# Kernel optimization log

Measured on AMD Instinct MI355X. Metric: run time of the kernel, lower is better.

## Reference

```python
import jax, jax.numpy as jnp
import numpy as np

B = 128; Hm = 13; Wm = 13; P = Hm * Wm; D = 256; TC = 32; RH = 512; EPS = 1e-5
START_TILE = 31


def _ln(x, g, b):
    m = jnp.mean(x, -1, keepdims=True)
    v = jnp.mean((x - m) ** 2, -1, keepdims=True)
    return (x - m) * jax.lax.rsqrt(v + EPS) * g + b


def _gelu(x):
    return jax.nn.gelu(x, approximate=False)


def _fwd(target_map, map_vec, mv_w, mv_b, tile_emb, row_emb, col_emb, pos_w, pos_b,
         c1_w, c1_b, bn1_g, bn1_b, c2_w, c2_b, bn2_g, bn2_b, patch_fc_w, patch_fc_b,
         qkv_w, qkv_b, out_w, out_b, ln1_g, ln1_b, ff1_w, ff1_b, ff2_w, ff2_b,
         ln2_g, ln2_b, gru_wih, gru_whh, gru_bih, gru_bhh,
         fc1_w, fc1_b, fcln_g, fcln_b, fc2_w, fc2_b):
    Bn = map_vec.shape[0]
    ys = jnp.arange(P) // Wm
    xs = jnp.arange(P) % Wm
    d5 = jnp.arange(5)
    # map_vec projection [B,256]
    mv = map_vec @ mv_w.T + mv_b
    # positional embedding for all 169 positions: cat(row_emb[y], col_emb[x]) -> fusion
    pos = jnp.concatenate([row_emb[ys], col_emb[xs]], -1) @ pos_w.T + pos_b  # [P,256]
    # teacher-forced previous tile (use_self_probility=0 path)
    tflat = target_map.reshape(Bn, P)
    prev = jnp.concatenate([jnp.full((Bn, 1), START_TILE, tflat.dtype), tflat[:, :-1]], 1)
    te = tile_emb[prev]  # [B,P,256]
    # 5x5 causal patches: rows y-4..y, cols x-2..x+2, out-of-bounds + current/future-on-row masked
    padded = jnp.pad(target_map, ((0, 0), (4, 0), (2, 2)))  # [B,17,17]
    rows = ys[:, None] + d5
    cols = xs[:, None] + d5
    patch = padded[:, rows[:, :, None], cols[:, None, :]]  # [B,P,5,5]
    vr = (ys[:, None, None] - 4 + d5[None, :, None]) >= 0
    oc = xs[:, None, None] - 2 + d5[None, None, :]
    vc = (oc >= 0) & (oc < Wm)
    mask = (vr & vc)
    mask = mask.at[:, 4, 2:].set(False)  # zero current cell and the two to its right
    patch = jnp.where(mask[None], patch, 0)
    oh = jax.nn.one_hot(patch, TC, dtype=jnp.float32)  # [B,P,row,col,c]
    # torch: permute(0,3,2,1) transposes the spatial dims of the one-hot channels
    ch = jnp.transpose(oh, (0, 1, 4, 3, 2))  # [B,P,32,col,row]
    mch = jnp.broadcast_to(mask.astype(jnp.float32)[None, :, None], (Bn, P, 1, 5, 5))
    x = jnp.concatenate([ch, mch], 2).reshape(Bn * P, TC + 1, 5, 5)
    dn = ('NCHW', 'OIHW', 'NCHW')
    bnsc = 1.0 / np.sqrt(1.0 + EPS)  # eval BN with running mean 0 / var 1
    x = jax.lax.conv_general_dilated(x, c1_w, (1, 1), 'SAME', dimension_numbers=dn) + c1_b[None, :, None, None]
    x = _gelu(x * (bn1_g * bnsc)[None, :, None, None] + bn1_b[None, :, None, None])
    x = jax.lax.conv_general_dilated(x, c2_w, (1, 1), 'VALID', dimension_numbers=dn) + c2_b[None, :, None, None]
    x = _gelu(x * (bn2_g * bnsc)[None, :, None, None] + bn2_b[None, :, None, None])
    pf = x.reshape(Bn * P, 128 * 9) @ patch_fc_w.T + patch_fc_b  # [B*P,256]
    # fusion transformer over 4 tokens, batched across all 169 steps
    tok = jnp.stack([
        te.reshape(Bn * P, D),
        jnp.broadcast_to(mv[:, None], (Bn, P, D)).reshape(Bn * P, D),
        jnp.broadcast_to(pos[None], (Bn, P, D)).reshape(Bn * P, D),
        pf], 1)  # [B*P,4,256]
    h = tok
    for l in range(3):  # post-norm encoder layers, relu FFN, dropout=0 at eval
        qkv = h @ qkv_w[l].T + qkv_b[l]
        q, k, v = jnp.split(qkv, 3, -1)
        hd = lambda t: t.reshape(-1, 4, 2, 128).transpose(0, 2, 1, 3)  # 2 heads of 128
        q, k, v = hd(q), hd(k), hd(v)
        a = jax.nn.softmax(jnp.einsum('nhqd,nhkd->nhqk', q, k) / np.sqrt(128.0), -1)
        o = jnp.einsum('nhqk,nhkd->nhqd', a, v).transpose(0, 2, 1, 3).reshape(-1, 4, D)
        h = _ln(h + o @ out_w[l].T + out_b[l], ln1_g[l], ln1_b[l])
        ff = jax.nn.relu(h @ ff1_w[l].T + ff1_b[l]) @ ff2_w[l].T + ff2_b[l]
        h = _ln(h + ff, ln2_g[l], ln2_b[l])
    feat = h[:, 0].reshape(Bn, P, D).transpose(1, 0, 2)  # [P,B,256]
    # GRUCell recurrence over the 169 raster steps
    gi = feat @ gru_wih.T + gru_bih  # [P,B,1536]

    def step(hid, g):
        gh = hid @ gru_whh.T + gru_bhh
        ir, iz, inn = jnp.split(g, 3, -1)
        hr, hz, hn = jnp.split(gh, 3, -1)
        r = jax.nn.sigmoid(ir + hr)
        z = jax.nn.sigmoid(iz + hz)
        n = jnp.tanh(inn + r * hn)
        hid = (1 - z) * n + z * hid
        return hid, hid

    _, hs = jax.lax.scan(step, jnp.zeros((Bn, RH), jnp.float32), gi)  # [P,B,512]
    hs = hs.transpose(1, 0, 2)  # [B,P,512]
    y = _gelu(_ln(hs @ fc1_w.T + fc1_b, fcln_g, fcln_b))
    logits = y @ fc2_w.T + fc2_b  # [B,P,32]
    return logits.reshape(Bn, Hm, Wm, TC).transpose(0, 3, 1, 2)  # [B,32,13,13]


def setup_inputs() -> dict:
    key = jax.random.key(0)
    ks = jax.random.split(key, 24)
    r = lambda i, s: jax.random.normal(ks[i], s, jnp.float32) * 0.02
    return {
        'map_vec': jax.random.normal(ks[0], (B, 32), jnp.float32),
        'target_map': jax.random.randint(ks[1], (B, Hm, Wm), 0, TC, jnp.int32),
        'mv_w': r(2, (256, 32)), 'mv_b': jnp.zeros(256),
        'tile_emb': r(3, (32, 256)),
        'row_emb': r(4, (13, 256)), 'col_emb': r(5, (13, 256)),
        'pos_w': r(6, (256, 512)), 'pos_b': jnp.zeros(256),
        'c1_w': r(7, (64, 33, 3, 3)), 'c1_b': jnp.zeros(64),
        'bn1_g': jnp.ones(64), 'bn1_b': jnp.zeros(64),
        'c2_w': r(8, (128, 64, 3, 3)), 'c2_b': jnp.zeros(128),
        'bn2_g': jnp.ones(128), 'bn2_b': jnp.zeros(128),
        'patch_fc_w': r(9, (256, 1152)), 'patch_fc_b': jnp.zeros(256),
        'qkv_w': r(10, (3, 768, 256)), 'qkv_b': jnp.zeros((3, 768)),
        'out_w': r(11, (3, 256, 256)), 'out_b': jnp.zeros((3, 256)),
        'ln1_g': jnp.ones((3, 256)), 'ln1_b': jnp.zeros((3, 256)),
        'ff1_w': r(12, (3, 256, 256)), 'ff1_b': jnp.zeros((3, 256)),
        'ff2_w': r(13, (3, 256, 256)), 'ff2_b': jnp.zeros((3, 256)),
        'ln2_g': jnp.ones((3, 256)), 'ln2_b': jnp.zeros((3, 256)),
        'gru_wih': r(14, (1536, 256)), 'gru_whh': r(15, (1536, 512)),
        'gru_bih': jnp.zeros(1536), 'gru_bhh': jnp.zeros(1536),
        'fc1_w': r(16, (512, 512)), 'fc1_b': jnp.zeros(512),
        'fcln_g': jnp.ones(512), 'fcln_b': jnp.zeros(512),
        'fc2_w': r(17, (32, 512)), 'fc2_b': jnp.zeros(32),
    }


def reference(map_vec, target_map, mv_w, mv_b, tile_emb, row_emb, col_emb, pos_w, pos_b,
              c1_w, c1_b, bn1_g, bn1_b, c2_w, c2_b, bn2_g, bn2_b, patch_fc_w, patch_fc_b,
              qkv_w, qkv_b, out_w, out_b, ln1_g, ln1_b, ff1_w, ff1_b, ff2_w, ff2_b,
              ln2_g, ln2_b, gru_wih, gru_whh, gru_bih, gru_bhh,
              fc1_w, fc1_b, fcln_g, fcln_b, fc2_w, fc2_b):
    return _fwd(target_map, map_vec, mv_w, mv_b, tile_emb, row_emb, col_emb, pos_w, pos_b,
                c1_w, c1_b, bn1_g, bn1_b, c2_w, c2_b, bn2_g, bn2_b, patch_fc_w, patch_fc_b,
                qkv_w, qkv_b, out_w, out_b, ln1_g, ln1_b, ff1_w, ff1_b, ff2_w, ff2_b,
                ln2_g, ln2_b, gru_wih, gru_whh, gru_bih, gru_bhh,
                fc1_w, fc1_b, fcln_g, fcln_b, fc2_w, fc2_b)
```

## Files before the change

### kernel.cpp

```cpp
#include <hip/hip_runtime.h>
#include <hip/hip_bf16.h>

typedef unsigned short u16;
typedef unsigned char u8;
typedef unsigned int u32;
typedef __attribute__((ext_vector_type(8))) short bf16x8;
typedef __attribute__((ext_vector_type(4))) float f32x4;
typedef __attribute__((ext_vector_type(4))) unsigned int u32x4;

__device__ __forceinline__ float us2f(u16 u){ return __uint_as_float(((unsigned)u)<<16); }
__device__ __forceinline__ u16 f2us(float f){
  __hip_bfloat16 h = __float2bfloat16(f);
  union { __hip_bfloat16 b; u16 s; } cv; cv.b = h; return cv.s;
}
__device__ __forceinline__ float gelu_f(float v){ return 0.5f*v*(1.f+erff(v*0.70710678118654752f)); }
__device__ __forceinline__ float sigm_f(float v){ return 1.f/(1.f+expf(-v)); }

#define BNSC 0.9999950000374997f

struct PrepArgs {
  const float *qkv_w, *out_w, *ff1_w, *ff2_w, *g_wih, *fc1_w, *pf_w, *c2_w, *fc2_w, *fc2_b;
  const float *c1_w, *c1_b, *bn2_g;
  const float *map_vec, *mv_w, *mv_b, *row_e, *col_e, *pos_w, *pos_b;
  const int *tm;
  u16 *qkvw_d, *outw_d, *ff1w_d, *ff2w_d, *wihw_d, *fc1w_d, *pfw_d, *w2k_d, *fc2w_d;
  float *fc2b_d, *w1t_d, *t2_d, *s2_d, *mv_d, *pos_d;
  u8 *ecls_d;
  unsigned *bar;
};
#define SB_QKV 2304
#define SB_O   768
#define SB_WIH 1536
#define SB_FC1 1024
#define SB_PF  1152
#define SB_W2  288
#define SB_FC2 128
#define SB_W1T 72
#define SB_T2  1057
#define SB_MV  128
#define SB_POS 169
#define SB_EC  2113
#define PREP_GRID (1+SB_QKV+3*SB_O+SB_WIH+SB_FC1+SB_PF+SB_W2+SB_FC2+SB_W1T+SB_T2+SB_MV+SB_POS+SB_EC)

__global__ __launch_bounds__(256) void prep_kernel(PrepArgs a){
  int bb = blockIdx.x; const int tid = threadIdx.x;
  if (bb < 1){
    if (tid < 64)  a.bar[tid] = 0u;
    if (tid < 128) a.s2_d[tid] = a.bn2_g[tid]*BNSC;
    return;
  } bb -= 1;
  if (bb < SB_QKV){ int i = bb*256+tid; a.qkvw_d[i] = f2us(a.qkv_w[i]); return; } bb -= SB_QKV;
  if (bb < SB_O){ int i = bb*256+tid; a.outw_d[i] = f2us(a.out_w[i]); return; } bb -= SB_O;
  if (bb < SB_O){ int i = bb*256+tid; a.ff1w_d[i] = f2us(a.ff1_w[i]); return; } bb -= SB_O;
  if (bb < SB_O){ int i = bb*256+tid; a.ff2w_d[i] = f2us(a.ff2_w[i]); return; } bb -= SB_O;
  if (bb < SB_WIH){ int i = bb*256+tid; a.wihw_d[i] = f2us(a.g_wih[i]); return; } bb -= SB_WIH;
  if (bb < SB_FC1){ int i = bb*256+tid; a.fc1w_d[i] = f2us(a.fc1_w[i]); return; } bb -= SB_FC1;
  if (bb < SB_PF){
    int i = bb*256+tid;
    int o = i/1152, kp = i%1152, pos = kp>>7, c = kp&127;
    a.pfw_d[i] = f2us(a.pf_w[o*1152 + c*9 + pos]); return;
  } bb -= SB_PF;
  if (bb < SB_W2){
    int i = bb*256+tid;
    int o = i/576, k = i%576, tap = k>>6, ic = k&63, ty = tap/3, tx = tap%3;
    a.w2k_d[i] = f2us(a.c2_w[((o*64 + ic)*3 + ty)*3 + tx]); return;
  } bb -= SB_W2;
  if (bb < SB_FC2){
    int i = bb*256+tid;
    int o = i>>9, k = i&511;
    a.fc2w_d[i] = (o<32) ? f2us(a.fc2_w[o*512+k]) : (u16)0;
    if (i < 64) a.fc2b_d[i] = (i<32) ? a.fc2_b[i] : 0.f;
    return;
  } bb -= SB_FC2;
  if (bb < SB_W1T){
    int i = bb*256+tid;
    int c = i/576, r = i%576, tap = r>>6, o = r&63;
    a.w1t_d[i] = a.c1_w[(o*33 + c)*9 + tap]; return;
  } bb -= SB_W1T;
  if (bb < SB_T2){
    int i = bb*256+tid; if (i >= 169*25*64) return;
    int blk = i/64, o = i%64;
    int p = blk/25, op = blk%25, oy = op/5, ox = op%5;
    int yp = p/13, xp = p%13;
    float acc = a.c1_b[o];
    for (int dy=0; dy<3; dy++) for (int dx=0; dx<3; dx++){
      int Y = oy+dy-1, X = ox+dx-1;
      if (Y<0||Y>4||X<0||X>4) continue;
      int rr = yp + Y - 4, cc = xp + X - 2;
      bool m = (rr>=0) && (cc>=0) && (cc<13) && !(Y==4 && X>=2);
      if (m) acc += a.c1_w[(o*33 + 32)*9 + dy*3 + dx];
    }
    a.t2_d[((long)p*25 + op)*64 + o] = acc; return;
  } bb -= SB_T2;
  if (bb < SB_MV){
    int i = bb*256+tid;
    int bi = i>>8, o = i&255;
    float acc = a.mv_b[o];
    for (int k=0;k<32;k++) acc += a.map_vec[bi*32+k]*a.mv_w[o*32+k];
    a.mv_d[i] = acc; return;
  } bb -= SB_MV;
  if (bb < SB_POS){
    int i = bb*256+tid;
    int p = i>>8, o = i&255;
    int y = p/13, x = p%13;
    const float* wr = a.pos_w + o*512;
    float acc = a.pos_b[o];
    for (int k=0;k<256;k++) acc += a.row_e[y*256+k]*wr[k];
    for (int k=0;k<256;k++) acc += a.col_e[x*256+k]*wr[256+k];
    a.pos_d[i] = acc; return;
  } bb -= SB_POS;
  {
    int id = bb*256+tid; if (id >= 21632*25) return;
    int n = id/25, q = id%25, Y = q/5, X = q%5;
    int b = n/169, p = n%169, yp = p/13, xp = p%13;
    int rr = yp + X - 4, cc = xp + Y - 2;
    int val = 0;
    if (rr>=0 && cc>=0 && cc<13 && !(X==4 && Y>=2)) val = a.tm[b*169 + rr*13 + cc];
    a.ecls_d[id] = (u8)val;
  }
}

__global__ __launch_bounds__(256) void conv1_kernel(
    const u8* __restrict__ ec, const float* __restrict__ w1t, const float* __restrict__ t2,
    const float* __restrict__ bn1g, const float* __restrict__ bn1b, u16* __restrict__ c1out,
    int nbase){
  __shared__ __align__(16) u16 w1s[32*9*64];
  __shared__ u8 ecs[32*25];
  const int tid = threadIdx.x, nl0 = blockIdx.x*32;
  for (int i=tid; i<32*9*64; i+=256) w1s[i] = f2us(w1t[i]);
  for (int i=tid; i<32*25;   i+=256) ecs[i] = ec[((long)nbase + nl0)*25 + i];
  __syncthreads();
  const int grp = tid>>6, o = tid&63;
  const float s1 = bn1g[o]*BNSC, t1 = bn1b[o];
  for (int it = grp; it < 800; it += 4){
    const int nl = it/25, op = it%25, oy = op/5, ox = op%5;
    const int n = nbase + nl0 + nl, p = n%169;
    float acc = t2[((long)p*25 + op)*64 + o];
    #pragma unroll
    for (int dy=0; dy<3; dy++)
      #pragma unroll
      for (int dx=0; dx<3; dx++){
        int Y = oy+dy-1, X = ox+dx-1;
        if (Y>=0 && Y<5 && X>=0 && X<5){
          int e = ecs[nl*25 + Y*5 + X];
          acc += us2f(w1s[(e*9 + dy*3+dx)*64 + o]);
        }
      }
    c1out[((long)(nl0+nl)*25 + op)*64 + o] = f2us(gelu_f(acc*s1 + t1));
  }
}

template<int NT, int OM>
__global__ __launch_bounds__(256) void gemm_bt(
    const u16* A, long lda, const u16* __restrict__ W,
    const float* __restrict__ bias,
    float* outF, u16* outB, long ldc, int N, int K, int act,
    const u16* __restrict__ lbase, const float* __restrict__ lg, const float* __restrict__ lb){
  __shared__ __align__(16) u16 As[64][72];
  __shared__ __align__(16) u16 Ws[NT][64][72];
  const int tid = threadIdx.x, wv = tid>>6, lane = tid&63;
  const int quad = lane>>4, l16 = lane&15;
  const int bm = blockIdx.y, bn = blockIdx.x;
  f32x4 acc[NT*4];
  #pragma unroll
  for (int i=0;i<NT*4;i++) acc[i] = (f32x4){0.f,0.f,0.f,0.f};
  const int sm = tid>>2, sk = (tid&3)<<4;
  const long arow = (long)(bm*64 + sm)*lda;
  for (int kb = 0; kb < K; kb += 64){
    int4 a0 = *(const int4*)(A + arow + kb + sk);
    int4 a1 = *(const int4*)(A + arow + kb + sk + 8);
    *(int4*)&As[sm][sk]   = a0;  *(int4*)&As[sm][sk+8] = a1;
    #pragma unroll
    for (int wt=0; wt<NT; wt++){
      const long wrow = (long)(bn*(64*NT) + wt*64 + sm)*K;
      int4 w0 = *(const int4*)(W + wrow + kb + sk);
      int4 w1 = *(const int4*)(W + wrow + kb + sk + 8);
      *(int4*)&Ws[wt][sm][sk]   = w0;  *(int4*)&Ws[wt][sm][sk+8] = w1;
    }
    __syncthreads();
    #pragma unroll
    for (int ks = 0; ks < 64; ks += 32){
      bf16x8 af = *(const bf16x8*)(&As[wv*16 + l16][ks + quad*8]);
      #pragma unroll
      for (int wt=0; wt<NT; wt++)
        #pragma unroll
        for (int s=0; s<4; s++){
          bf16x8 bfv = *(const bf16x8*)(&Ws[wt][s*16 + l16][ks + quad*8]);
          acc[wt*4+s] = __builtin_amdgcn_mfma_f32_16x16x32_bf16(af, bfv, acc[wt*4+s], 0, 0, 0);
        }
    }
    __syncthreads();
  }
  const int mb = bm*64 + wv*16 + quad*4;
  if (OM == 2){
    #pragma unroll
    for (int wt=0; wt<NT; wt++)
      #pragma unroll
      for (int s=0; s<4; s++){
        const int n = wt*64 + s*16 + l16;
        const float bv = bias[n];
        #pragma unroll
        for (int r=0;r<4;r++)
          acc[wt*4+s][r] = acc[wt*4+s][r] + bv + us2f(lbase[(long)(mb+r)*N + n]);
      }
    float mean[4], rstd[4];
    #pragma unroll
    for (int r=0;r<4;r++){
      float s = 0.f;
      #pragma unroll
      for (int i=0;i<NT*4;i++) s += acc[i][r];
      s += __shfl_xor(s,1); s += __shfl_xor(s,2); s += __shfl_xor(s,4); s += __shfl_xor(s,8);
      mean[r] = s / N;
      float v = 0.f;
      #pragma unroll
      for (int i=0;i<NT*4;i++){ float d = acc[i][r]-mean[r]; v += d*d; }
      v += __shfl_xor(v,1); v += __shfl_xor(v,2); v += __shfl_xor(v,4); v += __shfl_xor(v,8);
      rstd[r] = rsqrtf(v/N + 1e-5f);
    }
    #pragma unroll
    for (int wt=0; wt<NT; wt++)
      #pragma unroll
      for (int s=0; s<4; s++){
        const int n = wt*64 + s*16 + l16;
        const float gv = lg[n], bvv = lb[n];
        #pragma unroll
        for (int r=0;r<4;r++)
          outB[(long)(mb+r)*ldc + n] = f2us((acc[wt*4+s][r]-mean[r])*rstd[r]*gv + bvv);
      }
    return;
  }
  #pragma unroll
  for (int wt=0; wt<NT; wt++)
    #pragma unroll
    for (int s=0; s<4; s++){
      const int n = bn*(64*NT) + wt*64 + s*16 + l16;
      const float bv = bias ? bias[n] : 0.f;
      #pragma unroll
      for (int r=0;r<4;r++){
        float v = acc[wt*4+s][r] + bv;
        if (act==1) v = fmaxf(v, 0.f);
        else if (act==2) v = gelu_f(v);
        if (OM == 1){
          const int m = mb + r, b = m/169, tt = m%169;
          const int gate = n>>9, cblk = (n>>4)&31, jl = n&15;
          outB[(((long)tt*32 + cblk)*3 + gate)*2048 + b*16 + jl] = f2us(v);
        } else if (OM == 3){
          if (n < 32){
            const int m = mb + r, t = m/128, b2 = m%128;
            outF[((long)b2*32 + n)*169 + t] = v;
          }
        } else {
          const long oo = (long)(mb + r)*ldc + n;
          if (outF) outF[oo] = v;
          if (outB) outB[oo] = f2us(v);
        }
      }
    }
}

__global__ __launch_bounds__(256) void gemm_conv2(
    const u16* __restrict__ C1, const u16* __restrict__ W,
    const float* __restrict__ bias, const float* __restrict__ scale, const float* __restrict__ shift,
    u16* __restrict__ outB){
  __shared__ __align__(16) u16 As[64][72];
  __shared__ __align__(16) u16 Ws[64][72];
  const int tid = threadIdx.x, wv = tid>>6, lane = tid&63;
  const int quad = lane>>4, l16 = lane&15;
  const int bm = blockIdx.y, bn = blockIdx.x;
  f32x4 acc[4];
  #pragma unroll
  for (int i=0;i<4;i++) acc[i] = (f32x4){0.f,0.f,0.f,0.f};
  const int sm = tid>>2, sk = (tid&3)<<4;
  const int g = bm*64 + sm, n_ = g/9, pos = g%9, py = pos/3, px = pos%3;
  const long wrow = (long)(bn*64 + sm)*576;
  for (int tap = 0; tap < 9; tap++){
    const int kb = tap*64;
    const long aoff = ((long)n_*25 + (py + tap/3)*5 + (px + tap%3))*64 + sk;
    int4 a0 = *(const int4*)(C1 + aoff);
    int4 a1 = *(const int4*)(C1 + aoff + 8);
    int4 w0 = *(const int4*)(W + wrow + kb + sk);
    int4 w1 = *(const int4*)(W + wrow + kb + sk + 8);
    *(int4*)&As[sm][sk]   = a0;  *(int4*)&As[sm][sk+8] = a1;
    *(int4*)&Ws[sm][sk]   = w0;  *(int4*)&Ws[sm][sk+8] = w1;
    __syncthreads();
    #pragma unroll
    for (int ks = 0; ks < 64; ks += 32){
      bf16x8 af = *(const bf16x8*)(&As[wv*16 + l16][ks + quad*8]);
      #pragma unroll
      for (int nt=0; nt<4; nt++){
        bf16x8 bfv = *(const bf16x8*)(&Ws[nt*16 + l16][ks + quad*8]);
        acc[nt] = __builtin_amdgcn_mfma_f32_16x16x32_bf16(af, bfv, acc[nt], 0, 0, 0);
      }
    }
    __syncthreads();
  }
  const int mb = bm*64 + wv*16 + quad*4;
  #pragma unroll
  for (int nt=0; nt<4; nt++){
    const int n = bn*64 + nt*16 + l16;
    const float bv = bias[n], sc = scale[n], sh = shift[n];
    #pragma unroll
    for (int r=0;r<4;r++){
      float v = (acc[nt][r] + bv)*sc + sh;
      outB[(long)(mb + r)*128 + n] = f2us(gelu_f(v));
    }
  }
}

__global__ void token_kernel(const int* __restrict__ tm, const float* __restrict__ te,
                             const float* __restrict__ mv, const float* __restrict__ pos,
                             u16* __restrict__ hB){
  const int n = blockIdx.x, k = threadIdx.x;
  const int b = n/169, p = n%169;
  const int prev = (p==0) ? 31 : tm[b*169 + p - 1];
  const long r0 = (long)n*1024;
  hB[r0 + k]        = f2us(te[prev*256 + k]);
  hB[r0 + 256 + k]  = f2us(mv[b*256 + k]);
  hB[r0 + 512 + k]  = f2us(pos[p*256 + k]);
}

__global__ __launch_bounds__(256) void attn_kernel(const u16* __restrict__ qkv, u16* o){
  const int n = blockIdx.x*4 + (threadIdx.x>>6);
  const int lane = threadIdx.x & 63;
  float qv[4][2][2], kv[4][2][2], vv[4][2][2];
  #pragma unroll
  for (int tok=0; tok<4; tok++){
    const long rb = (long)(n*4+tok)*768;
    #pragma unroll
    for (int h=0; h<2; h++){
      unsigned u;
      u = *(const unsigned*)(qkv + rb +        h*128 + 2*lane); qv[tok][h][0]=us2f(u&0xffff); qv[tok][h][1]=us2f(u>>16);
      u = *(const unsigned*)(qkv + rb + 256 +  h*128 + 2*lane); kv[tok][h][0]=us2f(u&0xffff); kv[tok][h][1]=us2f(u>>16);
      u = *(const unsigned*)(qkv + rb + 512 +  h*128 + 2*lane); vv[tok][h][0]=us2f(u&0xffff); vv[tok][h][1]=us2f(u>>16);
    }
  }
  float sc[2][4][4];
  #pragma unroll
  for (int h=0; h<2; h++)
    #pragma unroll
    for (int qt=0; qt<4; qt++)
      #pragma unroll
      for (int kt=0; kt<4; kt++){
        float p_ = qv[qt][h][0]*kv[kt][h][0] + qv[qt][h][1]*kv[kt][h][1];
        for (int off=32; off; off>>=1) p_ += __shfl_xor(p_, off);
        sc[h][qt][kt] = p_ * 0.08838834764831845f;
      }
  #pragma unroll
  for (int h=0; h<2; h++)
    #pragma unroll
    for (int qt=0; qt<4; qt++){
      float m = fmaxf(fmaxf(sc[h][qt][0],sc[h][qt][1]),fmaxf(sc[h][qt][2],sc[h][qt][3]));
      float s = 0.f;
      #pragma unroll
      for (int kt=0; kt<4; kt++){ sc[h][qt][kt] = expf(sc[h][qt][kt]-m); s += sc[h][qt][kt]; }
      float inv = 1.f/s;
      #pragma unroll
      for (int kt=0; kt<4; kt++) sc[h][qt][kt] *= inv;
    }
  #pragma unroll
  for (int qt=0; qt<4; qt++)
    #pragma unroll
    for (int h=0; h<2; h++){
      float o0=0.f, o1=0.f;
      #pragma unroll
      for (int kt=0; kt<4; kt++){ o0 += sc[h][qt][kt]*vv[kt][h][0]; o1 += sc[h][qt][kt]*vv[kt][h][1]; }
      unsigned u = (unsigned)f2us(o0) | ((unsigned)f2us(o1)<<16);
      *(unsigned*)(o + (long)(n*4+qt)*256 + h*128 + 2*lane) = u;
    }
}

template<int NPL>
__global__ __launch_bounds__(256) void ln_kernel(
    const u16* __restrict__ delta, const u16* __restrict__ base,
    const float* __restrict__ g, const float* __restrict__ b,
    u16* __restrict__ out, int do_gelu){
  const int D = NPL*64;
  const int row = blockIdx.x*4 + (threadIdx.x>>6);
  const int lane = threadIdx.x & 63;
  const long ro = (long)row*D;
  float x[NPL];
  float s = 0.f;
  #pragma unroll
  for (int i=0;i<NPL;i++){
    float v = us2f(delta[ro + i*64 + lane]);
    if (base) v += us2f(base[ro + i*64 + lane]);
    x[i] = v; s += v;
  }
  for (int off=32; off; off>>=1) s += __shfl_xor(s, off);
  const float mean = s / D;
  float var = 0.f;
  #pragma unroll
  for (int i=0;i<NPL;i++){ float dd = x[i]-mean; var += dd*dd; }
  for (int off=32; off; off>>=1) var += __shfl_xor(var, off);
  const float rs = rsqrtf(var/D + 1e-5f);
  #pragma unroll
  for (int i=0;i<NPL;i++){
    float y = (x[i]-mean)*rs*g[i*64+lane] + b[i*64+lane];
    if (do_gelu) y = gelu_f(y);
    out[ro + i*64 + lane] = f2us(y);
  }
}

__global__ __launch_bounds__(256) void gru_kernel(
    const u16* __restrict__ gix, const float* __restrict__ whh,
    const float* __restrict__ bhh, u16* __restrict__ hx, u16* __restrict__ hs,
    unsigned* __restrict__ bar){
  __shared__ __align__(16) u16 Wl[48][520];
  __shared__ __align__(16) u16 hbuf[2048];
  const int c = blockIdx.x, tid = threadIdx.x;
  const int wv = tid>>6, lane = tid&63, quad = lane>>4, l16 = lane&15;
  for (int idx = tid; idx < 48*512; idx += 256){
    int g = idx >> 9, k = idx & 511;
    int gate = g >> 4, jl = g & 15;
    Wl[g][k] = f2us(whh[((gate<<9) + (c<<4) + jl)*512 + k]);
  }
  const int j = (c<<4) + l16;
  const float bh_r = bhh[j], bh_z = bhh[512+j], bh_n = bhh[1024+j];
  __syncthreads();
  float hold[2][4] = {{0.f,0.f,0.f,0.f},{0.f,0.f,0.f,0.f}};
  const int jlo = (quad&1)*8, jhiadd = quad>>1;
  for (int t=0; t<169; t++){
    const u16* gbase = gix + ((long)t*32 + c)*3*2048;
    float gr_[2][4], gz_[2][4], gn_[2][4];
    #pragma unroll
    for (int mt=0; mt<2; mt++)
      #pragma unroll
      for (int r=0; r<4; r++){
        const int b = (2*wv+mt)*16 + quad*4 + r;
        gr_[mt][r] = us2f(gbase[       b*16 + l16]);
        gz_[mt][r] = us2f(gbase[2048 + b*16 + l16]);
        gn_[mt][r] = us2f(gbase[4096 + b*16 + l16]);
      }
    if (t>0){
      if (tid==0){
        while (__hip_atomic_load(bar, __ATOMIC_RELAXED, __HIP_MEMORY_SCOPE_AGENT) < (unsigned)(32*t))
          __builtin_amdgcn_s_sleep(1);
      }
      __syncthreads();
    }
    f32x4 acc[2][3];
    #pragma unroll
    for (int mt=0; mt<2; mt++)
      #pragma unroll
      for (int g3=0; g3<3; g3++) acc[mt][g3] = (f32x4){0.f,0.f,0.f,0.f};
    if (t>0){
      const long tb = (long)(t-1)*65536;
      const int b0 = (2*wv+0)*16 + l16, b1 = (2*wv+1)*16 + l16;
      bf16x8 av0[16], av1[16];
      #pragma unroll
      for (int ii=0; ii<16; ii++){
        const long off = tb + (long)(ii*2 + jhiadd)*2048 + jlo;
        const u16* p0 = hx + off + b0*16;
        const u16* p1 = hx + off + b1*16;
        asm volatile("global_load_dwordx4 %0, %1, off sc0 sc1" : "=v"(av0[ii]) : "v"(p0));
        asm volatile("global_load_dwordx4 %0, %1, off sc0 sc1" : "=v"(av1[ii]) : "v"(p1));
      }
      asm volatile("s_waitcnt vmcnt(0)" ::: "memory");
      #pragma unroll
      for (int ii=0; ii<16; ii++){
        asm volatile("" : "+v"(av0[ii]));
        asm volatile("" : "+v"(av1[ii]));
      }
      #pragma unroll
      for (int ii=0; ii<16; ii++){
        const int ks = ii*32;
        #pragma unroll
        for (int g3=0; g3<3; g3++){
          bf16x8 bfv = *(const bf16x8*)(&Wl[g3*16 + l16][ks + quad*8]);
          acc[0][g3] = __builtin_amdgcn_mfma_f32_16x16x32_bf16(av0[ii], bfv, acc[0][g3], 0,0,0);
          acc[1][g3] = __builtin_amdgcn_mfma_f32_16x16x32_bf16(av1[ii], bfv, acc[1][g3], 0,0,0);
        }
      }
    }
    u16 hbv[2][4];
    #pragma unroll
    for (int mt=0; mt<2; mt++)
      #pragma unroll
      for (int r=0; r<4; r++){
        const int b = (2*wv+mt)*16 + quad*4 + r;
        float rr = sigm_f(gr_[mt][r] + acc[mt][0][r] + bh_r);
        float zz = sigm_f(gz_[mt][r] + acc[mt][1][r] + bh_z);
        float nn = tanhf (gn_[mt][r] + rr*(acc[mt][2][r] + bh_n));
        float h = (1.f-zz)*nn + zz*hold[mt][r];
        hold[mt][r] = h;
        hbv[mt][r] = f2us(h);
        hbuf[b*16 + l16] = hbv[mt][r];
      }
    __syncthreads();
    {
      u16* dst = hx + (long)t*65536 + c*2048 + tid*8;
      u32x4 val = *(const u32x4*)((const u32*)hbuf + tid*4);
      asm volatile("global_store_dwordx4 %0, %1, off sc0 sc1" :: "v"(dst), "v"(val) : "memory");
    }
    asm volatile("s_waitcnt vmcnt(0)" ::: "memory");
    __syncthreads();
    if (tid==0) __hip_atomic_fetch_add(bar, 1u, __ATOMIC_RELAXED, __HIP_MEMORY_SCOPE_AGENT);
    #pragma unroll
    for (int mt=0; mt<2; mt++)
      #pragma unroll
      for (int r=0; r<4; r++){
        const int b = (2*wv+mt)*16 + quad*4 + r;
        hs[((long)(t*128 + b))*512 + j] = hbv[mt][r];
      }
  }
}

extern "C" void kernel_launch(void* const* d_in, const int* in_sizes, int n_in,
                              void* d_out, int out_size, void* d_ws, size_t ws_size,
                              hipStream_t stream){
  (void)in_sizes; (void)n_in; (void)out_size;
  const float* map_vec = (const float*)d_in[0];
  const int*   tm      = (const int*)  d_in[1];
  const float* mv_w  = (const float*)d_in[2];
  const float* mv_b  = (const float*)d_in[3];
  const float* te    = (const float*)d_in[4];
  const float* row_e = (const float*)d_in[5];
  const float* col_e = (const float*)d_in[6];
  const float* pos_w = (const float*)d_in[7];
  const float* pos_b = (const float*)d_in[8];
  const float* c1_w  = (const float*)d_in[9];
  const float* c1_b  = (const float*)d_in[10];
  const float* bn1_g = (const float*)d_in[11];
  const float* bn1_b = (const float*)d_in[12];
  const float* c2_w  = (const float*)d_in[13];
  const float* c2_b  = (const float*)d_in[14];
  const float* bn2_g = (const float*)d_in[15];
  const float* bn2_b = (const float*)d_in[16];
  const float* pf_w  = (const float*)d_in[17];
  const float* pf_b  = (const float*)d_in[18];
  const float* qkv_w = (const float*)d_in[19];
  const float* qkv_b = (const float*)d_in[20];
  const float* out_w = (const float*)d_in[21];
  const float* out_b = (const float*)d_in[22];
  const float* ln1_g = (const float*)d_in[23];
  const float* ln1_b = (const float*)d_in[24];
  const float* ff1_w = (const float*)d_in[25];
  const float* ff1_b = (const float*)d_in[26];
  const float* ff2_w = (const float*)d_in[27];
  const float* ff2_b = (const float*)d_in[28];
  const float* ln2_g = (const float*)d_in[29];
  const float* ln2_b = (const float*)d_in[30];
  const float* g_wih = (const float*)d_in[31];
  const float* g_whh = (const float*)d_in[32];
  const float* g_bih = (const float*)d_in[33];
  const float* g_bhh = (const float*)d_in[34];
  const float* fc1_w = (const float*)d_in[35];
  const float* fc1_b = (const float*)d_in[36];
  const float* fln_g = (const float*)d_in[37];
  const float* fln_b = (const float*)d_in[38];
  const float* fc2_w = (const float*)d_in[39];
  const float* fc2_b = (const float*)d_in[40];

  char* ws = (char*)d_ws;
  constexpr size_t O_BAR  = 0;
  constexpr size_t O_QKVW = 256;
  constexpr size_t O_OUTW = O_QKVW + 1179648;
  constexpr size_t O_FF1W = O_OUTW + 393216;
  constexpr size_t O_FF2W = O_FF1W + 393216;
  constexpr size_t O_WIHW = O_FF2W + 393216;
  constexpr size_t O_FC1W = O_WIHW + 786432;
  constexpr size_t O_PFW  = O_FC1W + 524288;
  constexpr size_t O_W2K  = O_PFW  + 589824;
  constexpr size_t O_FC2W = O_W2K  + 147456;
  constexpr size_t O_FC2B = O_FC2W + 65536;
  constexpr size_t O_W1T  = O_FC2B + 256;
  constexpr size_t O_T2   = O_W1T  + 73728;
  constexpr size_t O_S2   = O_T2   + 1081600;
  constexpr size_t O_MV   = O_S2   + 512;
  constexpr size_t O_POS  = O_MV   + 131072;
  constexpr size_t O_ECLS = O_POS  + 173056;
  constexpr size_t O_R0   = ((O_ECLS + 540800 + 255)/256)*256;
  constexpr size_t R0_SZ  = 44302336;
  constexpr size_t O_R1   = O_R0 + R0_SZ;
  constexpr size_t R1_SZ  = 44302336;
  constexpr size_t O_R2   = O_R1 + R1_SZ;
  constexpr size_t R2_SZ  = 33226752;
  constexpr size_t ARENA_END = O_R2 + R2_SZ;
  if (ws_size < ARENA_END) return;
  const size_t O_HB    = O_R0;
  const size_t O_HX    = O_R0;
  const size_t O_HS    = O_R0 + 22151168;
  const size_t O_C1OUT = O_R1;
  const size_t O_OBUF  = O_R1;
  const size_t O_GIX   = O_R1;
  const size_t O_Y1    = O_R1;
  const size_t O_YB    = O_R1 + 22151168;
  const size_t O_C2OUT = O_R2;
  const size_t O_QKVC  = O_R2;

  PrepArgs pa;
  pa.qkv_w=qkv_w; pa.out_w=out_w; pa.ff1_w=ff1_w; pa.ff2_w=ff2_w; pa.g_wih=g_wih;
  pa.fc1_w=fc1_w; pa.pf_w=pf_w; pa.c2_w=c2_w; pa.fc2_w=fc2_w; pa.fc2_b=fc2_b;
  pa.c1_w=c1_w; pa.c1_b=c1_b; pa.bn2_g=bn2_g;
  pa.map_vec=map_vec; pa.mv_w=mv_w; pa.mv_b=mv_b; pa.row_e=row_e; pa.col_e=col_e;
  pa.pos_w=pos_w; pa.pos_b=pos_b; pa.tm=tm;
  pa.qkvw_d=(u16*)(ws+O_QKVW); pa.outw_d=(u16*)(ws+O_OUTW); pa.ff1w_d=(u16*)(ws+O_FF1W);
  pa.ff2w_d=(u16*)(ws+O_FF2W); pa.wihw_d=(u16*)(ws+O_WIHW); pa.fc1w_d=(u16*)(ws+O_FC1W);
  pa.pfw_d=(u16*)(ws+O_PFW); pa.w2k_d=(u16*)(ws+O_W2K); pa.fc2w_d=(u16*)(ws+O_FC2W);
  pa.fc2b_d=(float*)(ws+O_FC2B); pa.w1t_d=(float*)(ws+O_W1T); pa.t2_d=(float*)(ws+O_T2);
  pa.s2_d=(float*)(ws+O_S2); pa.mv_d=(float*)(ws+O_MV); pa.pos_d=(float*)(ws+O_POS);
  pa.ecls_d=(u8*)(ws+O_ECLS); pa.bar=(unsigned*)(ws+O_BAR);
  prep_kernel<<<PREP_GRID, 256, 0, stream>>>(pa);

  token_kernel<<<21632, 256, 0, stream>>>(tm, te, (const float*)(ws+O_MV), (const float*)(ws+O_POS),
      (u16*)(ws+O_HB));

  for (int cc = 0; cc < 2; cc++){
    const int nbase = cc*10816;
    conv1_kernel<<<338, 256, 0, stream>>>((const u8*)(ws+O_ECLS), (const float*)(ws+O_W1T),
        (const float*)(ws+O_T2), bn1_g, bn1_b, (u16*)(ws+O_C1OUT), nbase);
    gemm_conv2<<<dim3(2,1521), 256, 0, stream>>>((const u16*)(ws+O_C1OUT), (const u16*)(ws+O_W2K),
        c2_b, (const float*)(ws+O_S2), bn2_b, (u16*)(ws+O_C2OUT));
    gemm_bt<4,0><<<dim3(1,169), 256, 0, stream>>>((const u16*)(ws+O_C2OUT), 1152, (const u16*)(ws+O_PFW),
        pf_b, nullptr, (u16*)(ws+O_HB) + (size_t)nbase*1024 + 768, 1024, 256, 1152, 0,
        nullptr, nullptr, nullptr);
  }

  for (int l=0; l<3; l++){
    for (int cc = 0; cc < 4; cc++){
      gemm_bt<4,0><<<dim3(3,338), 256, 0, stream>>>((const u16*)(ws+O_HB) + (size_t)cc*21632*256, 256,
          (const u16*)(ws+O_QKVW) + (size_t)l*768*256, qkv_b + l*768,
          nullptr, (u16*)(ws+O_QKVC), 768, 768, 256, 0, nullptr, nullptr, nullptr);
      attn_kernel<<<1352, 256, 0, stream>>>((const u16*)(ws+O_QKVC),
          (u16*)(ws+O_OBUF) + (size_t)cc*5408*4*256);
    }
    gemm_bt<4,2><<<dim3(1,1352), 256, 0, stream>>>((const u16*)(ws+O_OBUF), 256,
        (const u16*)(ws+O_OUTW) + (size_t)l*256*256, out_b + l*256,
        nullptr, (u16*)(ws+O_HB), 256, 256, 256, 0,
        (const u16*)(ws+O_HB), ln1_g + l*256, ln1_b + l*256);
    gemm_bt<4,0><<<dim3(1,1352), 256, 0, stream>>>((const u16*)(ws+O_HB), 256,
        (const u16*)(ws+O_FF1W) + (size_t)l*256*256, ff1_b + l*256,
        nullptr, (u16*)(ws+O_OBUF), 256, 256, 256, 1, nullptr, nullptr, nullptr);
    gemm_bt<4,2><<<dim3(1,1352), 256, 0, stream>>>((const u16*)(ws+O_OBUF), 256,
        (const u16*)(ws+O_FF2W) + (size_t)l*256*256, ff2_b + l*256,
        nullptr, (u16*)(ws+O_HB), 256, 256, 256, 0,
        (const u16*)(ws+O_HB), ln2_g + l*256, ln2_b + l*256);
  }

  gemm_bt<4,1><<<dim3(6,338), 256, 0, stream>>>((const u16*)(ws+O_HB), 1024, (const u16*)(ws+O_WIHW),
      g_bih, nullptr, (u16*)(ws+O_GIX), 1536, 1536, 256, 0, nullptr, nullptr, nullptr);
  gru_kernel<<<32, 256, 0, stream>>>((const u16*)(ws+O_GIX), g_whh, g_bhh,
      (u16*)(ws+O_HX), (u16*)(ws+O_HS), (unsigned*)(ws+O_BAR));

  gemm_bt<4,0><<<dim3(2,338), 256, 0, stream>>>((const u16*)(ws+O_HS), 512, (const u16*)(ws+O_FC1W),
      fc1_b, nullptr, (u16*)(ws+O_Y1), 512, 512, 512, 0, nullptr, nullptr, nullptr);
  ln_kernel<8><<<5408, 256, 0, stream>>>((const u16*)(ws+O_Y1), nullptr, fln_g, fln_b,
      (u16*)(ws+O_YB), 1);
  gemm_bt<1,3><<<dim3(1,338), 256, 0, stream>>>((const u16*)(ws+O_YB), 512, (const u16*)(ws+O_FC2W),
      (const float*)(ws+O_FC2B), (float*)d_out, nullptr, 64, 64, 512, 0, nullptr, nullptr, nullptr);
}
```

Measured before the change: 2.921 ms.

## Use 128-row GEMM tiles and per-block flag barrier in GRU

Adds a gemm_bt2 variant that computes a 128x256 output tile per block (two M sub-tiles sharing each loaded weight fragment), halving grid size and weight reloads for the transformer, GRU input, and head GEMMs. The original gemm_bt is reduced to a plain bias-add kernel used only for the patch projection. The GRU inter-block barrier changes from a single atomic counter to per-block flag slots written with system-coherent stores and polled by 32 threads, which needs a larger zeroed barrier region. Larger tiles raise register pressure and may lower occupancy, and the flag protocol relies on cache-bypassing asm semantics.

```diff
diff --git a/kernel.cpp b/kernel.cpp
--- a/kernel.cpp
+++ b/kernel.cpp
@@ -45,7 +45,7 @@
 __global__ __launch_bounds__(256) void prep_kernel(PrepArgs a){
   int bb = blockIdx.x; const int tid = threadIdx.x;
   if (bb < 1){
-    if (tid < 64)  a.bar[tid] = 0u;
+    a.bar[tid] = 0u; a.bar[256+tid] = 0u;
     if (tid < 128) a.s2_d[tid] = a.bn2_g[tid]*BNSC;
     return;
   } bb -= 1;
@@ -150,12 +150,11 @@
   }
 }
 
-template<int NT, int OM>
+template<int NT>
 __global__ __launch_bounds__(256) void gemm_bt(
     const u16* A, long lda, const u16* __restrict__ W,
     const float* __restrict__ bias,
-    float* outF, u16* outB, long ldc, int N, int K, int act,
-    const u16* __restrict__ lbase, const float* __restrict__ lg, const float* __restrict__ lb){
+    u16* outB, long ldc, int N, int K){
   __shared__ __align__(16) u16 As[64][72];
   __shared__ __align__(16) u16 Ws[NT][64][72];
   const int tid = threadIdx.x, wv = tid>>6, lane = tid&63;
@@ -192,70 +191,139 @@
     __syncthreads();
   }
   const int mb = bm*64 + wv*16 + quad*4;
-  if (OM == 2){
-    #pragma unroll
-    for (int wt=0; wt<NT; wt++)
-      #pragma unroll
-      for (int s=0; s<4; s++){
-        const int n = wt*64 + s*16 + l16;
-        const float bv = bias[n];
-        #pragma unroll
-        for (int r=0;r<4;r++)
-          acc[wt*4+s][r] = acc[wt*4+s][r] + bv + us2f(lbase[(long)(mb+r)*N + n]);
-      }
-    float mean[4], rstd[4];
-    #pragma unroll
-    for (int r=0;r<4;r++){
-      float s = 0.f;
-      #pragma unroll
-      for (int i=0;i<NT*4;i++) s += acc[i][r];
-      s += __shfl_xor(s,1); s += __shfl_xor(s,2); s += __shfl_xor(s,4); s += __shfl_xor(s,8);
-      mean[r] = s / N;
-      float v = 0.f;
-      #pragma unroll
-      for (int i=0;i<NT*4;i++){ float d = acc[i][r]-mean[r]; v += d*d; }
-      v += __shfl_xor(v,1); v += __shfl_xor(v,2); v += __shfl_xor(v,4); v += __shfl_xor(v,8);
-      rstd[r] = rsqrtf(v/N + 1e-5f);
-    }
-    #pragma unroll
-    for (int wt=0; wt<NT; wt++)
-      #pragma unroll
-      for (int s=0; s<4; s++){
-        const int n = wt*64 + s*16 + l16;
-        const float gv = lg[n], bvv = lb[n];
-        #pragma unroll
-        for (int r=0;r<4;r++)
-          outB[(long)(mb+r)*ldc + n] = f2us((acc[wt*4+s][r]-mean[r])*rstd[r]*gv + bvv);
-      }
-    return;
-  }
   #pragma unroll
   for (int wt=0; wt<NT; wt++)
     #pragma unroll
     for (int s=0; s<4; s++){
       const int n = bn*(64*NT) + wt*64 + s*16 + l16;
-      const float bv = bias ? bias[n] : 0.f;
+      const float bv = bias[n];
+      #pragma unroll
+      for (int r=0;r<4;r++)
+        outB[(long)(mb + r)*ldc + n] = f2us(acc[wt*4+s][r] + bv);
+    }
+}
+
+template<int NT, int OM>
+__global__ __launch_bounds__(256) void gemm_bt2(
+    const u16* A, long lda, const u16* __restrict__ W,
+    const float* __restrict__ bias,
+    float* outF, u16* outB, long ldc, int N, int K, int act,
+    const u16* __restrict__ lbase, const float* __restrict__ lg, const float* __restrict__ lb){
+  __shared__ __align__(16) u16 As[128][72];
+  __shared__ __align__(16) u16 Ws[NT][64][72];
+  const int tid = threadIdx.x, wv = tid>>6, lane = tid&63;
+  const int quad = lane>>4, l16 = lane&15;
+  const int bm = blockIdx.y, bn = blockIdx.x;
+  f32x4 acc[2][NT*4];
+  #pragma unroll
+  for (int mt=0;mt<2;mt++)
+    #pragma unroll
+    for (int i=0;i<NT*4;i++) acc[mt][i] = (f32x4){0.f,0.f,0.f,0.f};
+  const int smA = tid>>1, skA = (tid&1)<<5;
+  const int smW = tid>>2, skW = (tid&3)<<4;
+  const long arow = (long)(bm*128 + smA)*lda;
+  for (int kb = 0; kb < K; kb += 64){
+    int4 a0 = *(const int4*)(A + arow + kb + skA);
+    int4 a1 = *(const int4*)(A + arow + kb + skA + 8);
+    int4 a2 = *(const int4*)(A + arow + kb + skA + 16);
+    int4 a3 = *(const int4*)(A + arow + kb + skA + 24);
+    *(int4*)&As[smA][skA]    = a0;  *(int4*)&As[smA][skA+8]  = a1;
+    *(int4*)&As[smA][skA+16] = a2;  *(int4*)&As[smA][skA+24] = a3;
+    #pragma unroll
+    for (int wt=0; wt<NT; wt++){
+      const long wrow = (long)(bn*(64*NT) + wt*64 + smW)*K;
+      int4 w0 = *(const int4*)(W + wrow + kb + skW);
+      int4 w1 = *(const int4*)(W + wrow + kb + skW + 8);
+      *(int4*)&Ws[wt][smW][skW]   = w0;  *(int4*)&Ws[wt][smW][skW+8] = w1;
+    }
+    __syncthreads();
+    #pragma unroll
+    for (int ks = 0; ks < 64; ks += 32){
+      bf16x8 af0 = *(const bf16x8*)(&As[wv*16 + l16][ks + quad*8]);
+      bf16x8 af1 = *(const bf16x8*)(&As[64 + wv*16 + l16][ks + quad*8]);
+      #pragma unroll
+      for (int wt=0; wt<NT; wt++)
+        #pragma unroll
+        for (int s=0; s<4; s++){
+          bf16x8 bfv = *(const bf16x8*)(&Ws[wt][s*16 + l16][ks + quad*8]);
+          acc[0][wt*4+s] = __builtin_amdgcn_mfma_f32_16x16x32_bf16(af0, bfv, acc[0][wt*4+s], 0, 0, 0);
+          acc[1][wt*4+s] = __builtin_amdgcn_mfma_f32_16x16x32_bf16(af1, bfv, acc[1][wt*4+s], 0, 0, 0);
+        }
+    }
+    __syncthreads();
+  }
+  if (OM == 2){
+    #pragma unroll
+    for (int mt=0; mt<2; mt++){
+      const int mb = bm*128 + mt*64 + wv*16 + quad*4;
+      #pragma unroll
+      for (int wt=0; wt<NT; wt++)
+        #pragma unroll
+        for (int s=0; s<4; s++){
+          const int n = wt*64 + s*16 + l16;
+          const float bv = bias[n];
+          #pragma unroll
+          for (int r=0;r<4;r++)
+            acc[mt][wt*4+s][r] = acc[mt][wt*4+s][r] + bv + us2f(lbase[(long)(mb+r)*N + n]);
+        }
+      float mean[4], rstd[4];
       #pragma unroll
       for (int r=0;r<4;r++){
-        float v = acc[wt*4+s][r] + bv;
-        if (act==1) v = fmaxf(v, 0.f);
-        else if (act==2) v = gelu_f(v);
-        if (OM == 1){
-          const int m = mb + r, b = m/169, tt = m%169;
-          const int gate = n>>9, cblk = (n>>4)&31, jl = n&15;
-          outB[(((long)tt*32 + cblk)*3 + gate)*2048 + b*16 + jl] = f2us(v);
-        } else if (OM == 3){
-          if (n < 32){
-            const int m = mb + r, t = m/128, b2 = m%128;
-            outF[((long)b2*32 + n)*169 + t] = v;
+        float s = 0.f;
+        #pragma unroll
+        for (int i=0;i<NT*4;i++) s += acc[mt][i][r];
+        s += __shfl_xor(s,1); s += __shfl_xor(s,2); s += __shfl_xor(s,4); s += __shfl_xor(s,8);
+        mean[r] = s / N;
+        float v = 0.f;
+        #pragma unroll
+        for (int i=0;i<NT*4;i++){ float d = acc[mt][i][r]-mean[r]; v += d*d; }
+        v += __shfl_xor(v,1); v += __shfl_xor(v,2); v += __shfl_xor(v,4); v += __shfl_xor(v,8);
+        rstd[r] = rsqrtf(v/N + 1e-5f);
+      }
+      #pragma unroll
+      for (int wt=0; wt<NT; wt++)
+        #pragma unroll
+        for (int s=0; s<4; s++){
+          const int n = wt*64 + s*16 + l16;
+          const float gv = lg[n], bvv = lb[n];
+          #pragma unroll
+          for (int r=0;r<4;r++)
+            outB[(long)(mb+r)*ldc + n] = f2us((acc[mt][wt*4+s][r]-mean[r])*rstd[r]*gv + bvv);
+        }
+    }
+    return;
+  }
+  #pragma unroll
+  for (int mt=0; mt<2; mt++){
+    const int mb = bm*128 + mt*64 + wv*16 + quad*4;
+    #pragma unroll
+    for (int wt=0; wt<NT; wt++)
+      #pragma unroll
+      for (int s=0; s<4; s++){
+        const int n = bn*(64*NT) + wt*64 + s*16 + l16;
+        const float bv = bias ? bias[n] : 0.f;
+        #pragma unroll
+        for (int r=0;r<4;r++){
+          float v = acc[mt][wt*4+s][r] + bv;
+          if (act==1) v = fmaxf(v, 0.f);
+          else if (act==2) v = gelu_f(v);
+          if (OM == 1){
+            const int m = mb + r, b = m/169, tt = m%169;
+            const int gate = n>>9, cblk = (n>>4)&31, jl = n&15;
+            outB[(((long)tt*32 + cblk)*3 + gate)*2048 + b*16 + jl] = f2us(v);
+          } else if (OM == 3){
+            if (n < 32){
+              const int m = mb + r, t = m/128, b2 = m%128;
+              outF[((long)b2*32 + n)*169 + t] = v;
+            }
+          } else {
+            const long oo = (long)(mb + r)*ldc + n;
+            if (outF) outF[oo] = v;
+            if (outB) outB[oo] = f2us(v);
           }
-        } else {
-          const long oo = (long)(mb + r)*ldc + n;
-          if (outF) outF[oo] = v;
-          if (outB) outB[oo] = f2us(v);
         }
       }
-    }
+  }
 }
 
 __global__ __launch_bounds__(256) void gemm_conv2(
@@ -432,9 +500,13 @@
         gn_[mt][r] = us2f(gbase[4096 + b*16 + l16]);
       }
     if (t>0){
-      if (tid==0){
-        while (__hip_atomic_load(bar, __ATOMIC_RELAXED, __HIP_MEMORY_SCOPE_AGENT) < (unsigned)(32*t))
-          __builtin_amdgcn_s_sleep(1);
+      if (tid < 32){
+        const u32* fp = bar + tid*16;
+        u32 v;
+        do {
+          asm volatile("global_load_dword %0, %1, off sc0 sc1" : "=v"(v) : "v"(fp));
+          asm volatile("s_waitcnt vmcnt(0)" ::: "memory");
+        } while ((int)v < t);
       }
       __syncthreads();
     }
@@ -494,7 +566,11 @@
     }
     asm volatile("s_waitcnt vmcnt(0)" ::: "memory");
     __syncthreads();
-    if (tid==0) __hip_atomic_fetch_add(bar, 1u, __ATOMIC_RELAXED, __HIP_MEMORY_SCOPE_AGENT);
+    if (tid==0){
+      u32 tv = (u32)(t+1);
+      const u32* fp = bar + c*16;
+      asm volatile("global_store_dword %0, %1, off sc0 sc1" :: "v"(fp), "v"(tv) : "memory");
+    }
     #pragma unroll
     for (int mt=0; mt<2; mt++)
       #pragma unroll
@@ -553,7 +629,7 @@
 
   char* ws = (char*)d_ws;
   constexpr size_t O_BAR  = 0;
-  constexpr size_t O_QKVW = 256;
+  constexpr size_t O_QKVW = 2048;
   constexpr size_t O_OUTW = O_QKVW + 1179648;
   constexpr size_t O_FF1W = O_OUTW + 393216;
   constexpr size_t O_FF2W = O_FF1W + 393216;
@@ -611,41 +687,40 @@
         (const float*)(ws+O_T2), bn1_g, bn1_b, (u16*)(ws+O_C1OUT), nbase);
     gemm_conv2<<<dim3(2,1521), 256, 0, stream>>>((const u16*)(ws+O_C1OUT), (const u16*)(ws+O_W2K),
         c2_b, (const float*)(ws+O_S2), bn2_b, (u16*)(ws+O_C2OUT));
-    gemm_bt<4,0><<<dim3(1,169), 256, 0, stream>>>((const u16*)(ws+O_C2OUT), 1152, (const u16*)(ws+O_PFW),
-        pf_b, nullptr, (u16*)(ws+O_HB) + (size_t)nbase*1024 + 768, 1024, 256, 1152, 0,
-        nullptr, nullptr, nullptr);
+    gemm_bt<4><<<dim3(1,169), 256, 0, stream>>>((const u16*)(ws+O_C2OUT), 1152, (const u16*)(ws+O_PFW),
+        pf_b, (u16*)(ws+O_HB) + (size_t)nbase*1024 + 768, 1024, 256, 1152);
   }
 
   for (int l=0; l<3; l++){
     for (int cc = 0; cc < 4; cc++){
-      gemm_bt<4,0><<<dim3(3,338), 256, 0, stream>>>((const u16*)(ws+O_HB) + (size_t)cc*21632*256, 256,
+      gemm_bt2<4,0><<<dim3(3,169), 256, 0, stream>>>((const u16*)(ws+O_HB) + (size_t)cc*21632*256, 256,
           (const u16*)(ws+O_QKVW) + (size_t)l*768*256, qkv_b + l*768,
           nullptr, (u16*)(ws+O_QKVC), 768, 768, 256, 0, nullptr, nullptr, nullptr);
       attn_kernel<<<1352, 256, 0, stream>>>((const u16*)(ws+O_QKVC),
           (u16*)(ws+O_OBUF) + (size_t)cc*5408*4*256);
     }
-    gemm_bt<4,2><<<dim3(1,1352), 256, 0, stream>>>((const u16*)(ws+O_OBUF), 256,
+    gemm_bt2<4,2><<<dim3(1,676), 256, 0, stream>>>((const u16*)(ws+O_OBUF), 256,
         (const u16*)(ws+O_OUTW) + (size_t)l*256*256, out_b + l*256,
         nullptr, (u16*)(ws+O_HB), 256, 256, 256, 0,
         (const u16*)(ws+O_HB), ln1_g + l*256, ln1_b + l*256);
-    gemm_bt<4,0><<<dim3(1,1352), 256, 0, stream>>>((const u16*)(ws+O_HB), 256,
+    gemm_bt2<4,0><<<dim3(1,676), 256, 0, stream>>>((const u16*)(ws+O_HB), 256,
         (const u16*)(ws+O_FF1W) + (size_t)l*256*256, ff1_b + l*256,
         nullptr, (u16*)(ws+O_OBUF), 256, 256, 256, 1, nullptr, nullptr, nullptr);
-    gemm_bt<4,2><<<dim3(1,1352), 256, 0, stream>>>((const u16*)(ws+O_OBUF), 256,
+    gemm_bt2<4,2><<<dim3(1,676), 256, 0, stream>>>((const u16*)(ws+O_OBUF), 256,
         (const u16*)(ws+O_FF2W) + (size_t)l*256*256, ff2_b + l*256,
         nullptr, (u16*)(ws+O_HB), 256, 256, 256, 0,
         (const u16*)(ws+O_HB), ln2_g + l*256, ln2_b + l*256);
   }
 
-  gemm_bt<4,1><<<dim3(6,338), 256, 0, stream>>>((const u16*)(ws+O_HB), 1024, (const u16*)(ws+O_WIHW),
+  gemm_bt2<4,1><<<dim3(6,169), 256, 0, stream>>>((const u16*)(ws+O_HB), 1024, (const u16*)(ws+O_WIHW),
       g_bih, nullptr, (u16*)(ws+O_GIX), 1536, 1536, 256, 0, nullptr, nullptr, nullptr);
   gru_kernel<<<32, 256, 0, stream>>>((const u16*)(ws+O_GIX), g_whh, g_bhh,
       (u16*)(ws+O_HX), (u16*)(ws+O_HS), (unsigned*)(ws+O_BAR));
 
-  gemm_bt<4,0><<<dim3(2,338), 256, 0, stream>>>((const u16*)(ws+O_HS), 512, (const u16*)(ws+O_FC1W),
+  gemm_bt2<4,0><<<dim3(2,169), 256, 0, stream>>>((const u16*)(ws+O_HS), 512, (const u16*)(ws+O_FC1W),
       fc1_b, nullptr, (u16*)(ws+O_Y1), 512, 512, 512, 0, nullptr, nullptr, nullptr);
   ln_kernel<8><<<5408, 256, 0, stream>>>((const u16*)(ws+O_Y1), nullptr, fln_g, fln_b,
       (u16*)(ws+O_YB), 1);
-  gemm_bt<1,3><<<dim3(1,338), 256, 0, stream>>>((const u16*)(ws+O_YB), 512, (const u16*)(ws+O_FC2W),
+  gemm_bt2<1,3><<<dim3(1,169), 256, 0, stream>>>((const u16*)(ws+O_YB), 512, (const u16*)(ws+O_FC2W),
       (const float*)(ws+O_FC2B), (float*)d_out, nullptr, 64, 64, 512, 0, nullptr, nullptr, nullptr);
 }
```

Result: slower. 3.365 ms (+15.2%).
